# Kernel optimization log

Measured on AMD Instinct MI355X. Metric: run time of the kernel, lower is better.

Reference implementation:

```python
import jax, jax.numpy as jnp
import numpy as np

B, T, I, H, D = 4, 4096, 1024, 16, 64


def setup_inputs() -> dict:
    key = jax.random.key(0)
    k1, k2, k3 = jax.random.split(key, 3)
    inputs = jax.random.normal(k1, (B, T, I), dtype=jnp.float32)
    kv_kernel = jax.random.normal(k2, (I, H, D, 2), dtype=jnp.float32) * (1.0 / np.sqrt(I))
    q_kernel = jax.random.normal(k3, (H, D), dtype=jnp.float32) * (1.0 / np.sqrt(D))
    return {"inputs": inputs, "kv_kernel": kv_kernel, "q_kernel": q_kernel}


def _combine(a, b):
    # state layout along last axis: [m (1), u (1), w (D)]
    ma, ua, wa = a[..., :1], a[..., 1:2], a[..., 2:]
    mb, ub, wb = b[..., :1], b[..., 1:2], b[..., 2:]
    m = jnp.maximum(ma, mb)
    ea = jnp.exp(ma - m)
    eb = jnp.exp(mb - m)
    return jnp.concatenate([m, ua * ea + ub * eb, wa * ea + wb * eb], axis=-1)


def reference(inputs, kv_kernel, q_kernel):
    # inputs: (B,T,I); kv_kernel: (I,H,D,2); q_kernel: (H,D)
    kv = jnp.einsum('bti,ihdk->bthdk', inputs, kv_kernel)
    kv = jax.nn.silu(kv)
    k = kv[..., 0]  # (B,T,H,D)
    v = kv[..., 1]  # (B,T,H,D)
    st = jnp.einsum('hd,bthd->bth', q_kernel, k)[..., None]  # (B,T,H,1)
    u_init = jnp.ones_like(st)
    elems = jnp.concatenate([st, u_init, v], axis=-1)  # (B,T,H,2+D)
    o = jax.lax.associative_scan(_combine, elems, axis=1)
    c = o[..., 1:2]  # denominator (B,T,H,1)
    a = o[..., 2:]   # numerator   (B,T,H,D)
    h = a / c        # (B,T,H,D)
    # concat_heads=False -> mean over heads
    return jnp.mean(h, axis=-2)  # (B,T,D)
```

## Files before the change

### kernel.cpp

```cpp
#include <hip/hip_runtime.h>
#include <hip/hip_bf16.h>
#include <math.h>

constexpr int B_ = 4, T_ = 4096, I_ = 1024, H_ = 16, D_ = 64;
constexpr int M_ = B_ * T_;
constexpr int N_ = H_ * D_ * 2;
constexpr int C_ = 64;
constexpr int L_ = T_ / C_;
constexpr int NT_ = 16;

typedef __bf16 bf16x8 __attribute__((ext_vector_type(8)));
typedef float  f32x4  __attribute__((ext_vector_type(4)));

__device__ __forceinline__ float silu_f(float x) {
    return x / (1.0f + __expf(-x));
}

__device__ __forceinline__ ushort f2bf_u(float x) {
    unsigned u = __float_as_uint(x);
    unsigned r = (u + 0x7fffu + ((u >> 16) & 1u)) >> 16;
    return (ushort)r;
}
__device__ __forceinline__ float bfu2f(ushort u) {
    return __uint_as_float(((unsigned)u) << 16);
}

__device__ __forceinline__ void gload_lds16(const void* g, void* l) {
    __builtin_amdgcn_global_load_lds(
        (const __attribute__((address_space(1))) unsigned int*)g,
        (__attribute__((address_space(3))) unsigned int*)l, 16, 0, 0);
}

__global__ __launch_bounds__(256) void convert_fused_kernel(
    const float* __restrict__ A,  ushort* __restrict__ A2,
    const float* __restrict__ Bm, ushort* __restrict__ B2T)
{
    __shared__ float tile[64][65];
    const int tid = threadIdx.x;
    if (blockIdx.x < 16384) {
        int idx = blockIdx.x * 256 + tid;
        int m  = idx >> 8;
        int kq = (idx & 255) * 4;
        float4 a = *reinterpret_cast<const float4*>(&A[(size_t)m * 1024 + kq]);
        ushort4 hi;
        hi.x = f2bf_u(a.x);
        hi.y = f2bf_u(a.y);
        hi.z = f2bf_u(a.z);
        hi.w = f2bf_u(a.w);
        *reinterpret_cast<ushort4*>(&A2[(size_t)m * 1024 + kq]) = hi;
    } else {
        int bk = blockIdx.x - 16384;
        const int k0 = (bk & 15) * 64;
        const int n0 = (bk >> 4) * 64;
        #pragma unroll
        for (int p = 0; p < 4; ++p) {
            int f = tid + p * 256;
            int r  = f >> 4;
            int c4 = (f & 15) * 4;
            float4 v = *reinterpret_cast<const float4*>(
                &Bm[(size_t)(k0 + r) * 2048 + n0 + c4]);
            tile[r][c4 + 0] = v.x; tile[r][c4 + 1] = v.y;
            tile[r][c4 + 2] = v.z; tile[r][c4 + 3] = v.w;
        }
        __syncthreads();
        #pragma unroll
        for (int p = 0; p < 4; ++p) {
            int f = tid + p * 256;
            int n  = f >> 4;
            int kq = (f & 15) * 4;
            ushort4 hi;
            hi.x = f2bf_u(tile[kq + 0][n]);
            hi.y = f2bf_u(tile[kq + 1][n]);
            hi.z = f2bf_u(tile[kq + 2][n]);
            hi.w = f2bf_u(tile[kq + 3][n]);
            *reinterpret_cast<ushort4*>(&B2T[(size_t)(n0 + n) * 1024 + k0 + kq]) = hi;
        }
    }
}

__device__ __forceinline__ int akof(int t) { return t * 64; }
__device__ __forceinline__ int bkof(int t) { return t * 64; }

#define BARRIER do { asm volatile("" ::: "memory"); \
    __builtin_amdgcn_s_barrier(); \
    asm volatile("" ::: "memory"); } while (0)
#define WAITLGKM asm volatile("s_waitcnt lgkmcnt(0)" ::: "memory")
#define WAITVM(n) asm volatile("s_waitcnt vmcnt(" #n ")" ::: "memory")

#define STAGE(gptr, kb, ldsoff, rs2) do { \
    gload_lds16((gptr) + (kb),         lds + (ldsoff) + tid * 8); \
    gload_lds16((gptr) + (kb) + (rs2), lds + (ldsoff) + 4096 + tid * 8); \
} while (0)

#define RDA(ab, i, kk) (*reinterpret_cast<const bf16x8*>((ab) + (i) * 1024 + ((kk) ? ck1 : ck0)))
#define RDB(bb, j, kk) (*reinterpret_cast<const bf16x8*>((bb) + (j) * 1024 + ((kk) ? ck1 : ck0)))

#define PH_READ_A(ab, ibase) do { \
    _Pragma("unroll") for (int i_ = 0; i_ < 4; ++i_) { \
        a[i_][0] = RDA(ab, (ibase) + i_, 0); \
        a[i_][1] = RDA(ab, (ibase) + i_, 1); } } while (0)
#define PH_READ_B(bb, breg, jbase) do { \
    _Pragma("unroll") for (int j_ = 0; j_ < 2; ++j_) { \
        breg[j_][0] = RDB(bb, (jbase) + j_, 0); \
        breg[j_][1] = RDB(bb, (jbase) + j_, 1); } } while (0)

#define QUAD(IH, BREG, JB) do { \
    __builtin_amdgcn_s_setprio(1); \
    _Pragma("unroll") for (int i_ = 0; i_ < 4; ++i_) \
    _Pragma("unroll") for (int j_ = 0; j_ < 2; ++j_) \
    _Pragma("unroll") for (int k_ = 0; k_ < 2; ++k_) \
        acc[(IH) + i_][(JB) + j_] = __builtin_amdgcn_mfma_f32_16x16x32_bf16( \
            a[i_][k_], BREG[j_][k_], acc[(IH) + i_][(JB) + j_], 0, 0, 0); \
    __builtin_amdgcn_s_setprio(0); \
} while (0)

__global__ __launch_bounds__(512, 2) void gemm_mfma8_kernel(
    const ushort* __restrict__ A2,
    const ushort* __restrict__ B2T,
    const float* __restrict__ qk,
    ushort* __restrict__ v_buf,
    float* __restrict__ s_buf,
    float* __restrict__ agg_m,
    float* __restrict__ agg_u,
    float* __restrict__ agg_w)
{
    __shared__ ushort lds[65536];
    __shared__ float spart[8][128];
    __shared__ float s_lds[2][256];

    const int bid = blockIdx.x;
    const int swz = (bid & 7) * 64 + (bid >> 3);
    const int bx  = swz >> 6;
    const int by  = swz & 63;
    const int m0  = by * 256;
    const int n0  = bx * 256;

    const int tid  = threadIdx.x;
    const int lane = tid & 63;
    const int wid  = tid >> 6;
    const int wr = wid >> 2, wc = wid & 3;
    const int l15 = lane & 15, lg = lane >> 4;

    const int row0 = tid >> 3;
    const int ch0  = (tid & 7) ^ (row0 & 7);
    const ushort* pA  = A2  + (size_t)(m0 + row0) * 1024 + ch0 * 8;
    const ushort* pB  = B2T + (size_t)(n0 + row0) * 1024 + ch0 * 8;
    const ushort* pA1 = pA + 128 * 1024;
    const ushort* pB1 = pB + 128 * 1024;

    const int ck0 = ((0 + lg) ^ (l15 & 7)) * 8;
    const int ck1 = ((4 + lg) ^ (l15 & 7)) * 8;
    const ushort* aB0 = lds + (wr * 128 + l15) * 64;
    const ushort* bB0 = lds + 16384 + (wc * 64 + l15) * 64;
    const ushort* aB1 = aB0 + 32768;
    const ushort* bB1 = bB0 + 32768;

    f32x4 acc[8][4];
    #pragma unroll
    for (int i = 0; i < 8; ++i)
        #pragma unroll
        for (int j = 0; j < 4; ++j)
            acc[i][j] = (f32x4){0.f, 0.f, 0.f, 0.f};
    bf16x8 a[4][2], b01[2][2], b23[2][2];

    {
        STAGE(pA,  akof(0), 0,             65536);
        STAGE(pA1, akof(0), 8192,          65536);
        STAGE(pB,  bkof(0), 16384,         65536);
        STAGE(pB1, bkof(0), 16384 + 8192,  65536);
        STAGE(pB,  bkof(1), 49152,         65536);
        STAGE(pA,  akof(1), 32768,         65536);
        WAITVM(4);
        BARRIER;
    }

    #pragma unroll 1
    for (int I = 0; I < NT_ / 2 - 1; ++I) {
        const int t1g = 2 * I + 1, t2g = 2 * I + 2, t3g = 2 * I + 3;
        const int ak1 = akof(t1g), bk1 = bkof(t1g);
        const int ak2 = akof(t2g), bk2 = bkof(t2g);
        const int ak3 = akof(t3g), bk3 = bkof(t3g);
        PH_READ_A(aB0, 0); PH_READ_B(bB0, b01, 0);
        STAGE(pA1, ak1, 32768 + 8192, 65536);
        BARRIER; WAITLGKM; QUAD(0, b01, 0); BARRIER;
        PH_READ_B(bB0, b23, 2);
        STAGE(pB1, bk1, 49152 + 8192, 65536);
        BARRIER; WAITLGKM; QUAD(0, b23, 2); BARRIER;
        PH_READ_A(aB0, 4);
        STAGE(pB, bk2, 16384, 65536);
        BARRIER; WAITLGKM; QUAD(4, b01, 0); BARRIER;
        STAGE(pA, ak2, 0, 65536);
        WAITVM(4);
        BARRIER; QUAD(4, b23, 2); BARRIER;
        PH_READ_A(aB1, 0); PH_READ_B(bB1, b01, 0);
        STAGE(pA1, ak2, 8192, 65536);
        BARRIER; WAITLGKM; QUAD(0, b01, 0); BARRIER;
        PH_READ_B(bB1, b23, 2);
        STAGE(pB1, bk2, 16384 + 8192, 65536);
        BARRIER; WAITLGKM; QUAD(0, b23, 2); BARRIER;
        PH_READ_A(aB1, 4);
        STAGE(pB, bk3, 49152, 65536);
        BARRIER; WAITLGKM; QUAD(4, b01, 0); BARRIER;
        STAGE(pA, ak3, 32768, 65536);
        WAITVM(4);
        BARRIER; QUAD(4, b23, 2); BARRIER;
    }

    {
        const int t1g = NT_ - 1;
        const int ak1 = akof(t1g), bk1 = bkof(t1g);
        PH_READ_A(aB0, 0); PH_READ_B(bB0, b01, 0);
        STAGE(pA1, ak1, 32768 + 8192, 65536);
        BARRIER; WAITLGKM; QUAD(0, b01, 0); BARRIER;
        PH_READ_B(bB0, b23, 2);
        STAGE(pB1, bk1, 49152 + 8192, 65536);
        BARRIER; WAITLGKM; QUAD(0, b23, 2); BARRIER;
        PH_READ_A(aB0, 4);
        BARRIER; WAITLGKM; QUAD(4, b01, 0); BARRIER;
        WAITVM(0);
        BARRIER; QUAD(4, b23, 2); BARRIER;
        PH_READ_A(aB1, 0); PH_READ_B(bB1, b01, 0);
        BARRIER; WAITLGKM; QUAD(0, b01, 0); BARRIER;
        PH_READ_B(bB1, b23, 2);
        BARRIER; WAITLGKM; QUAD(0, b23, 2); BARRIER;
        PH_READ_A(aB1, 4);
        BARRIER; WAITLGKM; QUAD(4, b01, 0); BARRIER;
        QUAD(4, b23, 2);
    }
    BARRIER;

    const int hloc  = wc >> 1;
    const int h     = 2 * bx + hloc;
    const int dbase = (wc & 1) * 32 + (l15 >> 1);
    float qv[4];
    #pragma unroll
    for (int j = 0; j < 4; ++j) qv[j] = qk[h * 64 + dbase + j * 8];
    const bool kcol = ((l15 & 1) == 0);

    #pragma unroll
    for (int i = 0; i < 8; ++i) {
        #pragma unroll
        for (int rr = 0; rr < 4; ++rr) {
            int rloc = wr * 128 + i * 16 + lg * 4 + rr;
            int m = m0 + rloc;
            int b = m >> 12, tt = m & 4095;
            float p = 0.f;
            #pragma unroll
            for (int j = 0; j < 4; ++j) {
                float sv = silu_f(acc[i][j][rr]);
                if (kcol) {
                    p += qv[j] * sv;
                } else {
                    ushort vb = f2bf_u(sv);
                    v_buf[((size_t)(b * H_ + h) * T_ + tt) * D_ + dbase + j * 8] = vb;
                    lds[hloc * 16384 + rloc * 64 + dbase + j * 8] = vb;
                }
            }
            p += __shfl_xor(p, 2);
            p += __shfl_xor(p, 4);
            p += __shfl_xor(p, 8);
            if (l15 == 0) spart[wid][i * 16 + lg * 4 + rr] = p;
        }
    }
    __syncthreads();
    {
        int wr2 = tid >> 8, hl = (tid >> 7) & 1, row = tid & 127;
        int m = m0 + wr2 * 128 + row;
        int b = m >> 12, tt = m & 4095;
        float sval = spart[wr2 * 4 + hl * 2][row] + spart[wr2 * 4 + hl * 2 + 1][row];
        s_buf[(size_t)(b * H_ + 2 * bx + hl) * T_ + tt] = sval;
        s_lds[hl][wr2 * 128 + row] = sval;
    }
    __syncthreads();

    {
        const int h_l = wid & 1;
        const int c_l = wid >> 1;
        const int b   = m0 >> 12;
        const int hg  = 2 * bx + h_l;
        const int cg  = ((m0 & 4095) >> 6) + c_l;
        const int base = (b * H_ + hg) * C_ + cg;
        const ushort* vl = lds + h_l * 16384 + (c_l * 64) * 64 + lane;
        const float*  sl = &s_lds[h_l][c_l * 64];
        float m = -INFINITY, u = 0.f, w = 0.f;
        #pragma unroll 8
        for (int t = 0; t < 64; ++t) {
            float s  = sl[t];
            float vv = bfu2f(vl[t * 64]);
            float mn = fmaxf(m, s);
            float ea = __expf(m - mn);
            float eb = __expf(s - mn);
            u = u * ea + eb;
            w = w * ea + vv * eb;
            m = mn;
        }
        if (lane == 0) { agg_m[base] = m; agg_u[base] = u; }
        agg_w[(size_t)base * D_ + lane] = w;
    }
}

#define TILE_M 128
#define TILE_N 128
#define TILE_K 16
__global__ __launch_bounds__(256) void gemm_kv_kernel(
    const float* __restrict__ A, const float* __restrict__ Bm,
    const float* __restrict__ q, ushort* __restrict__ v_buf,
    float* __restrict__ s_buf)
{
    __shared__ float As[TILE_K][TILE_M + 4];
    __shared__ float Bs[TILE_K][TILE_N + 4];
    const int tid = threadIdx.x;
    const int h   = blockIdx.x;
    const int bm  = blockIdx.y;
    const int m0  = bm * TILE_M;
    const int n0  = h * TILE_N;
    const int tx = tid & 15, ty = tid >> 4;
    float acc[8][8];
    #pragma unroll
    for (int i = 0; i < 8; ++i)
        #pragma unroll
        for (int j = 0; j < 8; ++j) acc[i][j] = 0.f;
    for (int k0 = 0; k0 < I_; k0 += TILE_K) {
        #pragma unroll
        for (int p = 0; p < 2; ++p) {
            int f = tid + p * 256;
            int row = f >> 2, kq = (f & 3) * 4;
            float4 av = *reinterpret_cast<const float4*>(
                &A[(size_t)(m0 + row) * I_ + k0 + kq]);
            As[kq + 0][row] = av.x; As[kq + 1][row] = av.y;
            As[kq + 2][row] = av.z; As[kq + 3][row] = av.w;
        }
        #pragma unroll
        for (int p = 0; p < 2; ++p) {
            int f = tid + p * 256;
            int row = f >> 5, c4 = (f & 31) * 4;
            *reinterpret_cast<float4*>(&Bs[row][c4]) =
                *reinterpret_cast<const float4*>(
                    &Bm[(size_t)(k0 + row) * N_ + n0 + c4]);
        }
        __syncthreads();
        #pragma unroll
        for (int kk = 0; kk < TILE_K; ++kk) {
            float4 a0 = *reinterpret_cast<const float4*>(&As[kk][ty * 8]);
            float4 a1 = *reinterpret_cast<const float4*>(&As[kk][ty * 8 + 4]);
            float4 b0 = *reinterpret_cast<const float4*>(&Bs[kk][tx * 8]);
            float4 b1 = *reinterpret_cast<const float4*>(&Bs[kk][tx * 8 + 4]);
            float af[8] = {a0.x, a0.y, a0.z, a0.w, a1.x, a1.y, a1.z, a1.w};
            float bf[8] = {b0.x, b0.y, b0.z, b0.w, b1.x, b1.y, b1.z, b1.w};
            #pragma unroll
            for (int i = 0; i < 8; ++i)
                #pragma unroll
                for (int j = 0; j < 8; ++j)
                    acc[i][j] = fmaf(af[i], bf[j], acc[i][j]);
        }
        __syncthreads();
    }
    float4 qv = *reinterpret_cast<const float4*>(&q[h * D_ + tx * 4]);
    float qf[4] = {qv.x, qv.y, qv.z, qv.w};
    #pragma unroll
    for (int i = 0; i < 8; ++i) {
        int m = m0 + ty * 8 + i;
        int b = m >> 12, t = m & 4095;
        float partial = 0.f;
        #pragma unroll
        for (int j = 0; j < 4; ++j) {
            float kval = silu_f(acc[i][2 * j]);
            float vv = silu_f(acc[i][2 * j + 1]);
            v_buf[((size_t)(b * H_ + h) * T_ + t) * D_ + tx * 4 + j] = f2bf_u(vv);
            partial = fmaf(qf[j], kval, partial);
        }
        #pragma unroll
        for (int mask = 8; mask >= 1; mask >>= 1)
            partial += __shfl_xor(partial, mask, 16);
        if (tx == 0) s_buf[(size_t)(b * H_ + h) * T_ + t] = partial;
    }
}

__global__ __launch_bounds__(64) void chunk_agg_kernel(
    const float* __restrict__ s_buf, const ushort* __restrict__ v_buf,
    float* __restrict__ agg_m, float* __restrict__ agg_u,
    float* __restrict__ agg_w)
{
    const int x    = blockIdx.x;
    const int c    = x & (C_ - 1);
    const int bh   = x >> 6;
    const int lane = threadIdx.x;
    const float* sp  = s_buf + (size_t)bh * T_ + c * L_;
    const ushort* vp = v_buf + ((size_t)bh * T_ + c * L_) * D_ + lane;
    float m = -INFINITY, u = 0.f, w = 0.f;
    for (int t = 0; t < L_; ++t) {
        float s  = sp[t];
        float vv = bfu2f(vp[(size_t)t * D_]);
        float mn = fmaxf(m, s);
        float ea = __expf(m - mn);
        float eb = __expf(s - mn);
        u = u * ea + eb;
        w = w * ea + vv * eb;
        m = mn;
    }
    if (lane == 0) { agg_m[x] = m; agg_u[x] = u; }
    agg_w[(size_t)x * D_ + lane] = w;
}

__global__ __launch_bounds__(64) void chunk_prefix_kernel(
    float* __restrict__ agg_m, float* __restrict__ agg_u,
    float* __restrict__ agg_w)
{
    const int bh   = blockIdx.x;
    const int lane = threadIdx.x;
    float pm = -INFINITY, pu = 0.f, pw = 0.f;
    #pragma unroll 4
    for (int c = 0; c < C_; ++c) {
        int base = bh * C_ + c;
        float am = agg_m[base];
        float au = agg_u[base];
        float aw = agg_w[(size_t)base * D_ + lane];
        if (lane == 0) { agg_m[base] = pm; agg_u[base] = pu; }
        agg_w[(size_t)base * D_ + lane] = pw;
        float mn = fmaxf(pm, am);
        float ea = __expf(pm - mn);
        float eb = __expf(am - mn);
        pu = pu * ea + au * eb;
        pw = pw * ea + aw * eb;
        pm = mn;
    }
}

__global__ __launch_bounds__(256) void scan_apply_kernel(
    const float* __restrict__ s_buf, const ushort* __restrict__ v_buf,
    const float* __restrict__ agg_m, const float* __restrict__ agg_u,
    const float* __restrict__ agg_w, float* __restrict__ out)
{
    __shared__ float part[4][8][64];
    const int bx   = blockIdx.x;
    const int b    = bx >> 6;
    const int c    = bx & (C_ - 1);
    const int w    = threadIdx.x >> 6;
    const int lane = threadIdx.x & 63;
    float m[4], u[4], ws[4];
    #pragma unroll
    for (int j = 0; j < 4; ++j) {
        int h = w * 4 + j;
        int base = (b * H_ + h) * C_ + c;
        m[j]  = agg_m[base];
        u[j]  = agg_u[base];
        ws[j] = agg_w[(size_t)base * D_ + lane];
    }
    const int t0 = c * L_;
    for (int g = 0; g < L_ / 8; ++g) {
        #pragma unroll
        for (int qq = 0; qq < 8; ++qq) {
            int t = t0 + g * 8 + qq;
            float acc = 0.f;
            #pragma unroll
            for (int j = 0; j < 4; ++j) {
                int h = w * 4 + j;
                size_t bht = (size_t)(b * H_ + h) * T_ + t;
                float s  = s_buf[bht];
                float vv = bfu2f(v_buf[bht * D_ + lane]);
                float mn = fmaxf(m[j], s);
                float ea = __expf(m[j] - mn);
                float eb = __expf(s - mn);
                u[j]  = u[j] * ea + eb;
                ws[j] = ws[j] * ea + vv * eb;
                m[j]  = mn;
                acc += ws[j] / u[j];
            }
            part[w][qq][lane] = acc;
        }
        __syncthreads();
        {
            int e  = threadIdx.x;
            int tt = e >> 6, d = e & 63;
            float sum = part[0][tt][d] + part[1][tt][d]
                      + part[2][tt][d] + part[3][tt][d];
            out[((size_t)b * T_ + (t0 + g * 8 + tt)) * D_ + d] = sum * (1.f / 16.f);
        }
        {
            int e  = threadIdx.x + 256;
            int tt = e >> 6, d = e & 63;
            float sum = part[0][tt][d] + part[1][tt][d]
                      + part[2][tt][d] + part[3][tt][d];
            out[((size_t)b * T_ + (t0 + g * 8 + tt)) * D_ + d] = sum * (1.f / 16.f);
        }
        __syncthreads();
    }
}

extern "C" void kernel_launch(void* const* d_in, const int* in_sizes, int n_in,
                              void* d_out, int out_size, void* d_ws, size_t ws_size,
                              hipStream_t stream) {
    const float* A  = (const float*)d_in[0];
    const float* Bm = (const float*)d_in[1];
    const float* q  = (const float*)d_in[2];
    float* out = (float*)d_out;

    ushort* v_buf = (ushort*)d_ws;
    float*  s_buf = (float*)(v_buf + (size_t)B_ * H_ * T_ * D_);
    float*  agg_m = s_buf + (size_t)B_ * H_ * T_;
    float*  agg_u = agg_m + B_ * H_ * C_;
    float*  agg_w = agg_u + B_ * H_ * C_;
    ushort* A2    = (ushort*)(agg_w + (size_t)B_ * H_ * C_ * D_);
    ushort* B2T   = A2 + (size_t)M_ * 1024;

    size_t need = (size_t)B_ * H_ * T_ * D_ * 2
                + ((size_t)262144 + 4096 + 4096 + 262144) * 4
                + ((size_t)M_ * 1024 + (size_t)2048 * 1024) * 2;

    if (ws_size >= need) {
        convert_fused_kernel<<<16896, 256, 0, stream>>>(A, A2, Bm, B2T);
        gemm_mfma8_kernel<<<512, 512, 0, stream>>>(A2, B2T, q, v_buf, s_buf,
                                                   agg_m, agg_u, agg_w);
    } else {
        dim3 ggrid(H_, M_ / TILE_M);
        gemm_kv_kernel<<<ggrid, 256, 0, stream>>>(A, Bm, q, v_buf, s_buf);
        chunk_agg_kernel<<<B_ * H_ * C_, 64, 0, stream>>>(s_buf, v_buf,
                                                          agg_m, agg_u, agg_w);
    }
    chunk_prefix_kernel<<<B_ * H_, 64, 0, stream>>>(agg_m, agg_u, agg_w);
    scan_apply_kernel<<<B_ * C_, 256, 0, stream>>>(s_buf, v_buf, agg_m, agg_u, agg_w, out);
}
```

Before: 161.0 us.

## Compute chunk scan aggregates directly from MFMA accumulators in registers

The per-chunk online-softmax aggregation now reads the v values straight from the GEMM accumulator registers, recomputing SiLU on them. Previously the bf16 v tile was written into LDS and then re-read one row at a time by a serial 64-step loop. Each lane folds its own rows, and partial states are merged across lanes with xor shuffles. This drops the LDS staging of v, one barrier, and the long serial loop, at the cost of redundant SiLU evaluations and extra shuffle and exp work. Aggregation now runs on fp32 v instead of bf16-rounded values, so results differ slightly.

```diff
diff --git a/kernel.cpp b/kernel.cpp
--- a/kernel.cpp
+++ b/kernel.cpp
@@ -227,7 +227,6 @@
         BARRIER; WAITLGKM; QUAD(4, b01, 0); BARRIER;
         QUAD(4, b23, 2);
     }
-    BARRIER;
 
     const int hloc  = wc >> 1;
     const int h     = 2 * bx + hloc;
@@ -251,9 +250,8 @@
                 if (kcol) {
                     p += qv[j] * sv;
                 } else {
-                    ushort vb = f2bf_u(sv);
-                    v_buf[((size_t)(b * H_ + h) * T_ + tt) * D_ + dbase + j * 8] = vb;
-                    lds[hloc * 16384 + rloc * 64 + dbase + j * 8] = vb;
+                    v_buf[((size_t)(b * H_ + h) * T_ + tt) * D_ + dbase + j * 8] =
+                        f2bf_u(sv);
                 }
             }
             p += __shfl_xor(p, 2);
@@ -274,28 +272,59 @@
     __syncthreads();
 
     {
-        const int h_l = wid & 1;
-        const int c_l = wid >> 1;
-        const int b   = m0 >> 12;
-        const int hg  = 2 * bx + h_l;
-        const int cg  = ((m0 & 4095) >> 6) + c_l;
-        const int base = (b * H_ + hg) * C_ + cg;
-        const ushort* vl = lds + h_l * 16384 + (c_l * 64) * 64 + lane;
-        const float*  sl = &s_lds[h_l][c_l * 64];
-        float m = -INFINITY, u = 0.f, w = 0.f;
-        #pragma unroll 8
-        for (int t = 0; t < 64; ++t) {
-            float s  = sl[t];
-            float vv = bfu2f(vl[t * 64]);
-            float mn = fmaxf(m, s);
-            float ea = __expf(m - mn);
-            float eb = __expf(s - mn);
-            u = u * ea + eb;
-            w = w * ea + vv * eb;
-            m = mn;
-        }
-        if (lane == 0) { agg_m[base] = m; agg_u[base] = u; }
-        agg_w[(size_t)base * D_ + lane] = w;
+        const int b  = m0 >> 12;
+        #pragma unroll
+        for (int cc = 0; cc < 2; ++cc) {
+            const int c_l = wr * 2 + cc;
+            const int cg  = ((m0 & 4095) >> 6) + c_l;
+            float mm = -INFINITY, u = 0.f;
+            float w0 = 0.f, w1 = 0.f, w2 = 0.f, w3 = 0.f;
+            #pragma unroll
+            for (int ir = 0; ir < 4; ++ir) {
+                #pragma unroll
+                for (int rr = 0; rr < 4; ++rr) {
+                    float s  = s_lds[hloc][c_l * 64 + ir * 16 + lg * 4 + rr];
+                    float mn = fmaxf(mm, s);
+                    float ea = __expf(mm - mn);
+                    float eb = __expf(s - mn);
+                    u  = u * ea + eb;
+                    w0 = w0 * ea + silu_f(acc[cc * 4 + ir][0][rr]) * eb;
+                    w1 = w1 * ea + silu_f(acc[cc * 4 + ir][1][rr]) * eb;
+                    w2 = w2 * ea + silu_f(acc[cc * 4 + ir][2][rr]) * eb;
+                    w3 = w3 * ea + silu_f(acc[cc * 4 + ir][3][rr]) * eb;
+                    mm = mn;
+                }
+            }
+            #pragma unroll
+            for (int mk = 16; mk <= 32; mk <<= 1) {
+                float om = __shfl_xor(mm, mk);
+                float ou = __shfl_xor(u,  mk);
+                float o0 = __shfl_xor(w0, mk);
+                float o1 = __shfl_xor(w1, mk);
+                float o2 = __shfl_xor(w2, mk);
+                float o3 = __shfl_xor(w3, mk);
+                float mn = fmaxf(mm, om);
+                float ea = __expf(mm - mn);
+                float eb = __expf(om - mn);
+                u  = u * ea + ou * eb;
+                w0 = w0 * ea + o0 * eb;
+                w1 = w1 * ea + o1 * eb;
+                w2 = w2 * ea + o2 * eb;
+                w3 = w3 * ea + o3 * eb;
+                mm = mn;
+            }
+            const int base = (b * H_ + h) * C_ + cg;
+            if ((wc & 1) == 0 && lane == 0) {
+                agg_m[base] = mm;
+                agg_u[base] = u;
+            }
+            if (!kcol && lg == 0) {
+                agg_w[(size_t)base * D_ + dbase + 0 ] = w0;
+                agg_w[(size_t)base * D_ + dbase + 8 ] = w1;
+                agg_w[(size_t)base * D_ + dbase + 16] = w2;
+                agg_w[(size_t)base * D_ + dbase + 24] = w3;
+            }
+        }
     }
 }
 
```

New measurement: 153.5 us. -4.6%, faster.
